# Kernel optimization log

Hardware: AMD Instinct MI355X
Metric: run time of the kernel (lower is better)

The kernel has to match this reference:

```python
import jax, jax.numpy as jnp
import numpy as np

NUM_HEADS = 12
HEAD_DIM = 64
SCALE = HEAD_DIM ** -0.5


def setup_inputs() -> dict:
    key = jax.random.key(0)
    ks = jax.random.split(key, 5)
    B, N, C = 8, 1024, 768
    x = jax.random.normal(ks[0], (B, N, C), dtype=jnp.float32)
    qkv_w = jax.random.normal(ks[1], (3 * C, C), dtype=jnp.float32) * (C ** -0.5)
    qkv_b = jax.random.normal(ks[2], (3 * C,), dtype=jnp.float32) * 0.02
    proj_w = jax.random.normal(ks[3], (C, C), dtype=jnp.float32) * (C ** -0.5)
    proj_b = jax.random.normal(ks[4], (C,), dtype=jnp.float32) * 0.02
    return {"x": x, "qkv_w": qkv_w, "qkv_b": qkv_b, "proj_w": proj_w, "proj_b": proj_b}


def reference(x, qkv_w, qkv_b, proj_w, proj_b):
    B, N, C = x.shape
    H, D = NUM_HEADS, HEAD_DIM
    # qkv projection: (B,N,3C) -> (3,B,H,N,D)
    qkv = (x @ qkv_w.T + qkv_b).reshape(B, N, 3, H, D).transpose(2, 0, 3, 1, 4)
    q, k, v = qkv[0], qkv[1], qkv[2]
    q = q * SCALE
    # full N x N attention scores, softmax over keys
    attn = jax.nn.softmax(jnp.einsum("bhnd,bhmd->bhnm", q, k), axis=-1)
    # Libragrad: detach the softmax map before multiplying with V
    attn = jax.lax.stop_gradient(attn)
    out = jnp.einsum("bhnm,bhmd->bhnd", attn, v)  # (B,H,N,D)
    out = out.transpose(0, 2, 1, 3).reshape(B, N, C)
    return out @ proj_w.T + proj_b
```

## Files before the change

### kernel.cpp

```cpp
#include <hip/hip_runtime.h>

#define NH 12
#define HD 64
#define BB 8
#define SEQ 1024
#define CD 768

typedef __bf16 bf16x8 __attribute__((ext_vector_type(8)));
typedef float f32x4 __attribute__((ext_vector_type(4)));

__device__ __forceinline__ unsigned short f2bf(float f) {
    unsigned int u = __float_as_uint(f);
    u = (u + 0x7fffu + ((u >> 16) & 1u)) >> 16;
    return (unsigned short)u;
}

__device__ __forceinline__ void gld_lds16(const unsigned short* g, unsigned short* l) {
    __builtin_amdgcn_global_load_lds(
        (const __attribute__((address_space(1))) unsigned int*)g,
        (__attribute__((address_space(3))) unsigned int*)l, 16, 0, 0);
}

#define N4_X 1572864
#define N4_W1 442368
#define N4_W2 147456
__global__ void cast_all(const float* __restrict__ x, const float* __restrict__ w1,
                         const float* __restrict__ w2,
                         unsigned short* __restrict__ ox, unsigned short* __restrict__ ow1,
                         unsigned short* __restrict__ ow2) {
    int i = blockIdx.x * blockDim.x + threadIdx.x;
    const float4* src;
    ushort4* dst;
    if (i < N4_X) {
        src = (const float4*)x + i; dst = (ushort4*)ox + i;
    } else if (i < N4_X + N4_W1) {
        src = (const float4*)w1 + (i - N4_X); dst = (ushort4*)ow1 + (i - N4_X);
    } else if (i < N4_X + N4_W1 + N4_W2) {
        src = (const float4*)w2 + (i - N4_X - N4_W1); dst = (ushort4*)ow2 + (i - N4_X - N4_W1);
    } else return;
    float4 f = *src;
    ushort4 o;
    o.x = f2bf(f.x); o.y = f2bf(f.y); o.z = f2bf(f.z); o.w = f2bf(f.w);
    *dst = o;
}

template<int MODE>
__global__ __launch_bounds__(256)
void gemm_bt(const unsigned short* __restrict__ A, const unsigned short* __restrict__ W,
             const float* __restrict__ bias,
             unsigned short* __restrict__ qb, unsigned short* __restrict__ kb,
             unsigned short* __restrict__ vb, float* __restrict__ fout,
             int M, int N, int K) {
    __shared__ __attribute__((aligned(16))) unsigned short As[128 * 32];
    __shared__ __attribute__((aligned(16))) unsigned short Bs[128 * 32];

    const int t    = threadIdx.x;
    const int bm0  = blockIdx.x * 128;
    const int bn0  = blockIdx.y * 128;
    const int wave = t >> 6;
    const int lane = t & 63;
    const int wm   = (wave >> 1) * 64;
    const int wn   = (wave & 1) * 64;
    const int col  = lane & 15;
    const int quad = lane >> 4;

    const int srow = t >> 2;
    const int scol = (t & 3) * 8;

    f32x4 acc[4][4];
#pragma unroll
    for (int i = 0; i < 4; i++)
#pragma unroll
        for (int j = 0; j < 4; j++) acc[i][j] = (f32x4){0.f, 0.f, 0.f, 0.f};

    for (int k0 = 0; k0 < K; k0 += 32) {
        __syncthreads();
        gld_lds16(A + (size_t)(bm0 + srow) * K + k0 + scol,      As + srow * 32 + scol);
        gld_lds16(A + (size_t)(bm0 + 64 + srow) * K + k0 + scol, As + (64 + srow) * 32 + scol);
        gld_lds16(W + (size_t)(bn0 + srow) * K + k0 + scol,      Bs + srow * 32 + scol);
        gld_lds16(W + (size_t)(bn0 + 64 + srow) * K + k0 + scol, Bs + (64 + srow) * 32 + scol);
        __syncthreads();

        bf16x8 af[4], bf[4];
#pragma unroll
        for (int mi = 0; mi < 4; mi++)
            af[mi] = *(const bf16x8*)(As + (wm + mi * 16 + col) * 32 + quad * 8);
#pragma unroll
        for (int ni = 0; ni < 4; ni++)
            bf[ni] = *(const bf16x8*)(Bs + (wn + ni * 16 + col) * 32 + quad * 8);
#pragma unroll
        for (int mi = 0; mi < 4; mi++)
#pragma unroll
            for (int ni = 0; ni < 4; ni++)
                acc[mi][ni] = __builtin_amdgcn_mfma_f32_16x16x32_bf16(
                    af[mi], bf[ni], acc[mi][ni], 0, 0, 0);
    }

#pragma unroll
    for (int mi = 0; mi < 4; mi++) {
#pragma unroll
        for (int ni = 0; ni < 4; ni++) {
            const int n = bn0 + wn + ni * 16 + col;
            const float bv = bias[n];
#pragma unroll
            for (int r = 0; r < 4; r++) {
                const int m = bm0 + wm + mi * 16 + quad * 4 + r;
                float val = acc[mi][ni][r] + bv;
                if (MODE == 0) {
                    const int tq  = n / 768;
                    const int rem = n - tq * 768;
                    const int h   = rem >> 6;
                    const int d   = rem & 63;
                    const int b   = m >> 10;
                    const int nq  = m & 1023;
                    const size_t dst = ((size_t)(b * NH + h) * SEQ + nq) * HD + d;
                    if (tq == 0)      qb[dst] = f2bf(val * 0.125f);
                    else if (tq == 1) kb[dst] = f2bf(val);
                    else              vb[dst] = f2bf(val);
                } else {
                    fout[(size_t)m * N + n] = val;
                }
            }
        }
    }
}

__global__ __launch_bounds__(256)
void transpose_v(const unsigned short* __restrict__ v,
                 unsigned short* __restrict__ vt) {
    __shared__ unsigned short tile[64 * 72];
    const int bh = blockIdx.x;
    const int st = blockIdx.y;
    const int t  = threadIdx.x;
    const int sr = t >> 2;
    const int sc = (t & 3) * 16;

    const unsigned short* src = v + ((size_t)bh * SEQ + st * 64 + sr) * HD + sc;
    *(uint4*)(tile + sr * 72 + sc)     = *(const uint4*)src;
    *(uint4*)(tile + sr * 72 + sc + 8) = *(const uint4*)(src + 8);
    __syncthreads();

    union { unsigned short us[16]; uint4 u4[2]; } tmp;
#pragma unroll
    for (int i = 0; i < 16; i++) {
        const int p    = sc + i;
        const int orig = (p & 3) * 16 + (p >> 2);
        tmp.us[i] = tile[orig * 72 + sr];
    }
    unsigned short* dst = vt + ((size_t)bh * HD + sr) * SEQ + st * 64 + sc;
    *(uint4*)dst       = tmp.u4[0];
    *(uint4*)(dst + 8) = tmp.u4[1];
}

__global__ __launch_bounds__(256, 3)
void attn_mfma(const unsigned short* __restrict__ qb,
               const unsigned short* __restrict__ kb,
               const unsigned short* __restrict__ vtb,
               unsigned short* __restrict__ ob) {
    __shared__ __attribute__((aligned(16))) unsigned short Ks[64 * 72];
    __shared__ __attribute__((aligned(16))) unsigned short VT[64 * 72];
    __shared__ __attribute__((aligned(16))) unsigned short Ps[128 * 76];

    const int t  = threadIdx.x;
    const int bh = blockIdx.x;
    const int qt = blockIdx.y;
    const size_t base  = (size_t)bh * SEQ * HD;
    const size_t vbase = (size_t)bh * HD * SEQ;

    const int sr = t >> 2;
    const int sc = (t & 3) * 16;

    const int wave = t >> 6;
    const int lane = t & 63;
    const int col  = lane & 15;
    const int quad = lane >> 4;

    bf16x8 aq[2][2];
#pragma unroll
    for (int u = 0; u < 2; u++) {
        const int q = qt * 128 + (2 * wave + u) * 16 + col;
        aq[u][0] = *(const bf16x8*)(qb + base + (size_t)q * HD + quad * 8);
        aq[u][1] = *(const bf16x8*)(qb + base + (size_t)q * HD + 32 + quad * 8);
    }

    float l_r[2][4];
#pragma unroll
    for (int u = 0; u < 2; u++)
#pragma unroll
        for (int r = 0; r < 4; r++) l_r[u][r] = 0.f;
    f32x4 accO[2][4];
#pragma unroll
    for (int u = 0; u < 2; u++)
#pragma unroll
        for (int di = 0; di < 4; di++) accO[u][di] = (f32x4){0.f, 0.f, 0.f, 0.f};

    const unsigned short* kp = kb + base + (size_t)sr * HD + sc;
    const unsigned short* vp = vtb + vbase + (size_t)sr * SEQ + sc;
    uint4 kr0 = *(const uint4*)kp,       kr1 = *(const uint4*)(kp + 8);
    uint4 vr0 = *(const uint4*)vp,       vr1 = *(const uint4*)(vp + 8);

    for (int kc = 0; kc < 16; kc++) {
        __syncthreads();
        *(uint4*)(Ks + sr * 72 + sc)     = kr0;
        *(uint4*)(Ks + sr * 72 + sc + 8) = kr1;
        *(uint4*)(VT + sr * 72 + sc)     = vr0;
        *(uint4*)(VT + sr * 72 + sc + 8) = vr1;
        __syncthreads();

        if (kc < 15) {
            const unsigned short* kn = kp + (size_t)(kc + 1) * 64 * HD;
            const unsigned short* vn = vp + (kc + 1) * 64;
            kr0 = *(const uint4*)kn; kr1 = *(const uint4*)(kn + 8);
            vr0 = *(const uint4*)vn; vr1 = *(const uint4*)(vn + 8);
        }

        f32x4 accS[2][4];
#pragma unroll
        for (int ni = 0; ni < 4; ni++) {
            bf16x8 bk0 = *(const bf16x8*)(Ks + (ni * 16 + col) * 72 + quad * 8);
            bf16x8 bk1 = *(const bf16x8*)(Ks + (ni * 16 + col) * 72 + 32 + quad * 8);
#pragma unroll
            for (int u = 0; u < 2; u++) {
                f32x4 z = (f32x4){0.f, 0.f, 0.f, 0.f};
                z = __builtin_amdgcn_mfma_f32_16x16x32_bf16(aq[u][0], bk0, z, 0, 0, 0);
                z = __builtin_amdgcn_mfma_f32_16x16x32_bf16(aq[u][1], bk1, z, 0, 0, 0);
                accS[u][ni] = z;
            }
        }

#pragma unroll
        for (int u = 0; u < 2; u++) {
            const int prow = (2 * wave + u) * 16;
#pragma unroll
            for (int r = 0; r < 4; r++) {
                float p0 = __expf(accS[u][0][r]);
                float p1 = __expf(accS[u][1][r]);
                float p2 = __expf(accS[u][2][r]);
                float p3 = __expf(accS[u][3][r]);
                l_r[u][r] += (p0 + p1) + (p2 + p3);
                uint2 pk;
                pk.x = ((unsigned)f2bf(p1) << 16) | f2bf(p0);
                pk.y = ((unsigned)f2bf(p3) << 16) | f2bf(p2);
                *(uint2*)(Ps + (prow + quad * 4 + r) * 76 + col * 4) = pk;
            }
        }

        bf16x8 ap[2][2];
#pragma unroll
        for (int u = 0; u < 2; u++) {
            const int prow = (2 * wave + u) * 16;
            ap[u][0] = *(const bf16x8*)(Ps + (prow + col) * 76 + quad * 8);
            ap[u][1] = *(const bf16x8*)(Ps + (prow + col) * 76 + 32 + quad * 8);
        }
#pragma unroll
        for (int di = 0; di < 4; di++) {
            bf16x8 bv0 = *(const bf16x8*)(VT + (di * 16 + col) * 72 + quad * 8);
            bf16x8 bv1 = *(const bf16x8*)(VT + (di * 16 + col) * 72 + 32 + quad * 8);
#pragma unroll
            for (int u = 0; u < 2; u++) {
                accO[u][di] = __builtin_amdgcn_mfma_f32_16x16x32_bf16(ap[u][0], bv0, accO[u][di], 0, 0, 0);
                accO[u][di] = __builtin_amdgcn_mfma_f32_16x16x32_bf16(ap[u][1], bv1, accO[u][di], 0, 0, 0);
            }
        }
    }

    const int b = bh / NH, h = bh - b * NH;
#pragma unroll
    for (int u = 0; u < 2; u++)
#pragma unroll
        for (int r = 0; r < 4; r++) {
            float s = l_r[u][r];
            s += __shfl_xor(s, 1);
            s += __shfl_xor(s, 2);
            s += __shfl_xor(s, 4);
            s += __shfl_xor(s, 8);
            const float inv = 1.f / s;
            const int q = qt * 128 + (2 * wave + u) * 16 + quad * 4 + r;
            const size_t rowbase = ((size_t)b * SEQ + q) * CD + h * 64;
#pragma unroll
            for (int di = 0; di < 4; di++)
                ob[rowbase + di * 16 + col] = f2bf(accO[u][di][r] * inv);
        }
}

extern "C" void kernel_launch(void* const* d_in, const int* in_sizes, int n_in,
                              void* d_out, int out_size, void* d_ws, size_t ws_size,
                              hipStream_t stream) {
    const float* x      = (const float*)d_in[0];
    const float* qkv_w  = (const float*)d_in[1];
    const float* qkv_b  = (const float*)d_in[2];
    const float* proj_w = (const float*)d_in[3];
    const float* proj_b = (const float*)d_in[4];
    float* out = (float*)d_out;

    char* ws = (char*)d_ws;
    unsigned short* x_bf     = (unsigned short*)ws;
    unsigned short* vt_bf    = x_bf;
    unsigned short* qkvw_bf  = (unsigned short*)(ws + 12582912);
    unsigned short* projw_bf = (unsigned short*)(ws + 12582912 + 3538944);
    unsigned short* q_bf     = (unsigned short*)(ws + 12582912 + 3538944 + 1179648);
    unsigned short* k_bf     = q_bf + 6291456;
    unsigned short* v_bf     = k_bf + 6291456;
    unsigned short* attn_bf  = v_bf;

    cast_all<<<8448, 256, 0, stream>>>(x, qkv_w, proj_w, x_bf, qkvw_bf, projw_bf);

    gemm_bt<0><<<dim3(64, 18), 256, 0, stream>>>(x_bf, qkvw_bf, qkv_b,
                                                 q_bf, k_bf, v_bf, nullptr,
                                                 8192, 2304, 768);

    transpose_v<<<dim3(96, 16), 256, 0, stream>>>(v_bf, vt_bf);

    attn_mfma<<<dim3(96, 8), 256, 0, stream>>>(q_bf, k_bf, vt_bf, attn_bf);

    gemm_bt<1><<<dim3(64, 6), 256, 0, stream>>>(attn_bf, projw_bf, proj_b,
                                                nullptr, nullptr, nullptr, out,
                                                8192, 768, 768);
}
```

Measured before the change: 212.5 us.

## Fuse V transpose into attention LDS staging and simplify QKV epilogue addressing

Removes the separate transpose_v kernel; the attention kernel now loads V in its natural row-major layout and scatters it transposed into LDS with scalar 16-bit stores, using a permuted column position. The QKV GEMM epilogue now computes the destination buffer, scale, batch and head once per block tile instead of dividing and branching per element. The intent is to save a kernel launch and a full global read and write of V, at the cost of many narrow, potentially bank-conflicting LDS stores inside the attention loop.

Result: faster. 202.8 us (-4.6%).

```diff
diff --git a/kernel.cpp b/kernel.cpp
--- a/kernel.cpp
+++ b/kernel.cpp
@@ -96,66 +96,51 @@
                     af[mi], bf[ni], acc[mi][ni], 0, 0, 0);
     }
 
-#pragma unroll
-    for (int mi = 0; mi < 4; mi++) {
-#pragma unroll
-        for (int ni = 0; ni < 4; ni++) {
-            const int n = bn0 + wn + ni * 16 + col;
-            const float bv = bias[n];
+    if (MODE == 1) {
+#pragma unroll
+        for (int mi = 0; mi < 4; mi++)
+#pragma unroll
+            for (int ni = 0; ni < 4; ni++) {
+                const int n = bn0 + wn + ni * 16 + col;
+                const float bv = bias[n];
+#pragma unroll
+                for (int r = 0; r < 4; r++) {
+                    const int m = bm0 + wm + mi * 16 + quad * 4 + r;
+                    fout[(size_t)m * N + n] = acc[mi][ni][r] + bv;
+                }
+            }
+        return;
+    }
+
+    const int sel = bn0 / 768;
+    const int nb  = bn0 - sel * 768;
+    const int b   = bm0 >> 10;
+    const int nqb = bm0 & 1023;
+    unsigned short* const dstbuf = (sel == 0) ? qb : (sel == 1) ? kb : vb;
+    const float scale = (sel == 0) ? 0.125f : 1.0f;
+
+#pragma unroll
+    for (int ni = 0; ni < 4; ni++) {
+        const int hn = nb + wn + ni * 16;
+        const int h  = hn >> 6;
+        const int d0 = hn & 63;
+        const float bv = bias[bn0 + wn + ni * 16 + col];
+        unsigned short* const rowbase =
+            dstbuf + ((size_t)(b * NH + h) * SEQ) * HD + d0 + col;
+#pragma unroll
+        for (int mi = 0; mi < 4; mi++)
 #pragma unroll
             for (int r = 0; r < 4; r++) {
-                const int m = bm0 + wm + mi * 16 + quad * 4 + r;
-                float val = acc[mi][ni][r] + bv;
-                if (MODE == 0) {
-                    const int tq  = n / 768;
-                    const int rem = n - tq * 768;
-                    const int h   = rem >> 6;
-                    const int d   = rem & 63;
-                    const int b   = m >> 10;
-                    const int nq  = m & 1023;
-                    const size_t dst = ((size_t)(b * NH + h) * SEQ + nq) * HD + d;
-                    if (tq == 0)      qb[dst] = f2bf(val * 0.125f);
-                    else if (tq == 1) kb[dst] = f2bf(val);
-                    else              vb[dst] = f2bf(val);
-                } else {
-                    fout[(size_t)m * N + n] = val;
-                }
-            }
-        }
-    }
-}
-
-__global__ __launch_bounds__(256)
-void transpose_v(const unsigned short* __restrict__ v,
-                 unsigned short* __restrict__ vt) {
-    __shared__ unsigned short tile[64 * 72];
-    const int bh = blockIdx.x;
-    const int st = blockIdx.y;
-    const int t  = threadIdx.x;
-    const int sr = t >> 2;
-    const int sc = (t & 3) * 16;
-
-    const unsigned short* src = v + ((size_t)bh * SEQ + st * 64 + sr) * HD + sc;
-    *(uint4*)(tile + sr * 72 + sc)     = *(const uint4*)src;
-    *(uint4*)(tile + sr * 72 + sc + 8) = *(const uint4*)(src + 8);
-    __syncthreads();
-
-    union { unsigned short us[16]; uint4 u4[2]; } tmp;
-#pragma unroll
-    for (int i = 0; i < 16; i++) {
-        const int p    = sc + i;
-        const int orig = (p & 3) * 16 + (p >> 2);
-        tmp.us[i] = tile[orig * 72 + sr];
-    }
-    unsigned short* dst = vt + ((size_t)bh * HD + sr) * SEQ + st * 64 + sc;
-    *(uint4*)dst       = tmp.u4[0];
-    *(uint4*)(dst + 8) = tmp.u4[1];
+                const int nq = nqb + wm + mi * 16 + quad * 4 + r;
+                rowbase[(size_t)nq * HD] = f2bf((acc[mi][ni][r] + bv) * scale);
+            }
+    }
 }
 
 __global__ __launch_bounds__(256, 3)
 void attn_mfma(const unsigned short* __restrict__ qb,
                const unsigned short* __restrict__ kb,
-               const unsigned short* __restrict__ vtb,
+               const unsigned short* __restrict__ vb,
                unsigned short* __restrict__ ob) {
     __shared__ __attribute__((aligned(16))) unsigned short Ks[64 * 72];
     __shared__ __attribute__((aligned(16))) unsigned short VT[64 * 72];
@@ -164,8 +149,7 @@
     const int t  = threadIdx.x;
     const int bh = blockIdx.x;
     const int qt = blockIdx.y;
-    const size_t base  = (size_t)bh * SEQ * HD;
-    const size_t vbase = (size_t)bh * HD * SEQ;
+    const size_t base = (size_t)bh * SEQ * HD;
 
     const int sr = t >> 2;
     const int sc = (t & 3) * 16;
@@ -195,21 +179,28 @@
         for (int di = 0; di < 4; di++) accO[u][di] = (f32x4){0.f, 0.f, 0.f, 0.f};
 
     const unsigned short* kp = kb + base + (size_t)sr * HD + sc;
-    const unsigned short* vp = vtb + vbase + (size_t)sr * SEQ + sc;
-    uint4 kr0 = *(const uint4*)kp,       kr1 = *(const uint4*)(kp + 8);
-    uint4 vr0 = *(const uint4*)vp,       vr1 = *(const uint4*)(vp + 8);
+    const unsigned short* vp = vb + base + (size_t)sr * HD + sc;
+    uint4 kr0 = *(const uint4*)kp,  kr1 = *(const uint4*)(kp + 8);
+    uint4 vr0 = *(const uint4*)vp,  vr1 = *(const uint4*)(vp + 8);
+
+    const int vpos = (sr & 15) * 4 + (sr >> 4);
 
     for (int kc = 0; kc < 16; kc++) {
         __syncthreads();
         *(uint4*)(Ks + sr * 72 + sc)     = kr0;
         *(uint4*)(Ks + sr * 72 + sc + 8) = kr1;
-        *(uint4*)(VT + sr * 72 + sc)     = vr0;
-        *(uint4*)(VT + sr * 72 + sc + 8) = vr1;
+        {
+            union { uint4 u4[2]; unsigned short us[16]; } vv;
+            vv.u4[0] = vr0; vv.u4[1] = vr1;
+#pragma unroll
+            for (int j = 0; j < 16; j++)
+                VT[(sc + j) * 72 + vpos] = vv.us[j];
+        }
         __syncthreads();
 
         if (kc < 15) {
             const unsigned short* kn = kp + (size_t)(kc + 1) * 64 * HD;
-            const unsigned short* vn = vp + (kc + 1) * 64;
+            const unsigned short* vn = vp + (size_t)(kc + 1) * 64 * HD;
             kr0 = *(const uint4*)kn; kr1 = *(const uint4*)(kn + 8);
             vr0 = *(const uint4*)vn; vr1 = *(const uint4*)(vn + 8);
         }
@@ -295,13 +286,12 @@
 
     char* ws = (char*)d_ws;
     unsigned short* x_bf     = (unsigned short*)ws;
-    unsigned short* vt_bf    = x_bf;
+    unsigned short* attn_bf  = x_bf;
     unsigned short* qkvw_bf  = (unsigned short*)(ws + 12582912);
     unsigned short* projw_bf = (unsigned short*)(ws + 12582912 + 3538944);
     unsigned short* q_bf     = (unsigned short*)(ws + 12582912 + 3538944 + 1179648);
     unsigned short* k_bf     = q_bf + 6291456;
     unsigned short* v_bf     = k_bf + 6291456;
-    unsigned short* attn_bf  = v_bf;
 
     cast_all<<<8448, 256, 0, stream>>>(x, qkv_w, proj_w, x_bf, qkvw_bf, projw_bf);
 
@@ -309,9 +299,7 @@
                                                  q_bf, k_bf, v_bf, nullptr,
                                                  8192, 2304, 768);
 
-    transpose_v<<<dim3(96, 16), 256, 0, stream>>>(v_bf, vt_bf);
-
-    attn_mfma<<<dim3(96, 8), 256, 0, stream>>>(q_bf, k_bf, vt_bf, attn_bf);
+    attn_mfma<<<dim3(96, 8), 256, 0, stream>>>(q_bf, k_bf, v_bf, attn_bf);
 
     gemm_bt<1><<<dim3(64, 6), 256, 0, stream>>>(attn_bf, projw_bf, proj_b,
                                                 nullptr, nullptr, nullptr, out,
```
